# Performance work log

Hardware: AMD Instinct MI355X
Metric: run time of the kernel (lower is better)

The kernel has to match this reference:

```python
import jax, jax.numpy as jnp
import numpy as np

N_NODES = 50000
N_EDGES = 800000
NFEAT = 128
NHID = 128


def gcn_conv(x, edge_index, W, b):
    """PyG GCNConv: add self-loops, symmetric deg^-1/2 normalization, scatter-add."""
    n = x.shape[0]
    loop = jnp.arange(n, dtype=edge_index.dtype)
    row = jnp.concatenate([edge_index[0], loop])  # source nodes
    col = jnp.concatenate([edge_index[1], loop])  # target nodes
    ones = jnp.ones(row.shape[0], dtype=x.dtype)
    deg = jax.ops.segment_sum(ones, col, num_segments=n)
    dinv = jnp.where(deg > 0, jax.lax.rsqrt(deg), 0.0).astype(x.dtype)
    norm = dinv[row] * dinv[col]  # [E+N]
    h = x @ W  # [n, out]
    msg = h[row] * norm[:, None]  # gather + scale, [E+N, out]
    out = jax.ops.segment_sum(msg, col, num_segments=n)  # scatter-add
    return out + b


def setup_inputs() -> dict:
    key = jax.random.key(0)
    kx, ke, k1, k2 = jax.random.split(key, 4)
    x = jax.random.normal(kx, (N_NODES, NFEAT), dtype=jnp.float32)
    edge_index = jax.random.randint(ke, (2, N_EDGES), 0, N_NODES, dtype=jnp.int32)
    s1 = 1.0 / np.sqrt(NFEAT)
    s2 = 1.0 / np.sqrt(NHID)
    W1 = jax.random.uniform(k1, (NFEAT, NHID), jnp.float32, -s1, s1)
    b1 = jnp.zeros((NHID,), jnp.float32)
    W2 = jax.random.uniform(k2, (NHID, NHID), jnp.float32, -s2, s2)
    b2 = jnp.zeros((NHID,), jnp.float32)
    return {"x": x, "edge_index": edge_index, "W1": W1, "b1": b1, "W2": W2, "b2": b2}


def reference(x, edge_index, W1, b1, W2, b2):
    # DGI.forward -> encoder z: relu(GCNConv) x2, dropout=0, no layernorm
    h = jax.nn.relu(gcn_conv(x, edge_index, W1, b1))
    z = jax.nn.relu(gcn_conv(h, edge_index, W2, b2))
    return z
```

## Files before the change

kernel.cpp:

```cpp
#include <hip/hip_runtime.h>
#include <hip/hip_fp16.h>


#define NBK 98
#define BSH 9
#define BCAP 10240
#define NBB 391

typedef _Float16 f16x8 __attribute__((ext_vector_type(8)));
typedef float f32x4 __attribute__((ext_vector_type(4)));

__global__ __launch_bounds__(256) void k_prep_bucket(
    const int* __restrict__ row, const int* __restrict__ col,
    int* __restrict__ bcur, unsigned int* __restrict__ arena, int E,
    const float* __restrict__ W1, const float* __restrict__ W2,
    __half* __restrict__ Wt1, __half* __restrict__ Wt2) {
  int tid = threadIdx.x;
  if (blockIdx.x >= NBB) {
    int i = (blockIdx.x - NBB) * 256 + tid;
    int n = i >> 7, k = i & 127;
    Wt1[i] = (__half)W1[k * 128 + n];
    Wt2[i] = (__half)W2[k * 128 + n];
    return;
  }
  __shared__ int hist[NBK];
  __shared__ int basec[NBK];
  if (tid < NBK) hist[tid] = 0;
  __syncthreads();
  int base = blockIdx.x * 2048;
  int cc[8], rr[8], bb[8];
#pragma unroll
  for (int j = 0; j < 8; ++j) {
    int e = base + j * 256 + tid;
    bb[j] = -1;
    if (e < E) {
      cc[j] = col[e];
      rr[j] = row[e];
      bb[j] = cc[j] >> BSH;
      atomicAdd(&hist[bb[j]], 1);
    }
  }
  __syncthreads();
  if (tid < NBK && hist[tid] > 0)
    basec[tid] = atomicAdd(&bcur[tid], hist[tid]);
  __syncthreads();
#pragma unroll
  for (int j = 0; j < 8; ++j) {
    if (bb[j] >= 0) {
      int pos = atomicAdd(&basec[bb[j]], 1);
      if (pos < BCAP)
        arena[(size_t)bb[j] * BCAP + pos] =
            ((unsigned int)rr[j] << BSH) | (unsigned int)(cc[j] & 511);
    }
  }
}

__global__ __launch_bounds__(256) void k_csr(const int* __restrict__ bcur,
                                             const unsigned int* __restrict__ arena,
                                             int* __restrict__ offs,
                                             float* __restrict__ dinv,
                                             int* __restrict__ esrc, int n) {
  __shared__ int hist[512];
  __shared__ int psum[256];
  int b = blockIdx.x, tid = threadIdx.x;
  hist[tid] = 0;
  hist[tid + 256] = 0;
  __syncthreads();
  int m = min(bcur[b], BCAP);
  const unsigned int* a = arena + (size_t)b * BCAP;
  for (int i = tid; i < m; i += 256) atomicAdd(&hist[a[i] & 511], 1);
  __syncthreads();

  psum[tid] = (tid < b && tid < NBK) ? min(bcur[tid], BCAP) : 0;
  __syncthreads();
#pragma unroll
  for (int d = 128; d > 0; d >>= 1) {
    if (tid < d) psum[tid] += psum[tid + d];
    __syncthreads();
  }
  int base = psum[0];
  __syncthreads();

  int a0 = hist[2 * tid], a1 = hist[2 * tid + 1];
  int pair = a0 + a1;
  psum[tid] = pair;
  __syncthreads();
#pragma unroll
  for (int d = 1; d < 256; d <<= 1) {
    int add = (tid >= d) ? psum[tid - d] : 0;
    __syncthreads();
    psum[tid] += add;
    __syncthreads();
  }
  int excl = psum[tid] - pair;
  int o0 = base + excl, o1 = o0 + a0;

  int nb0 = b << BSH;
  int node0 = nb0 + 2 * tid, node1 = node0 + 1;
  if (node0 < n) {
    offs[node0] = o0;
    dinv[node0] = rsqrtf((float)(a0 + 1));
  }
  if (node1 < n) {
    offs[node1] = o1;
    dinv[node1] = rsqrtf((float)(a1 + 1));
  }
  if (b == NBK - 1 && tid == 255) offs[n] = base + psum[255];
  __syncthreads();

  hist[2 * tid] = o0;
  hist[2 * tid + 1] = o1;
  __syncthreads();
  for (int i = tid; i < m; i += 256) {
    unsigned int p = a[i];
    int pos = atomicAdd(&hist[p & 511], 1);
    esrc[pos] = (int)(p >> BSH);
  }
}

__device__ inline uint4 loadA16(const float* A, int grow, int k16, int M) {
  if (grow >= M) return make_uint4(0, 0, 0, 0);
  const float4* p = (const float4*)(A + (size_t)grow * 128 + k16 * 8);
  float4 f0 = p[0], f1 = p[1];
  __half2 h0 = __floats2half2_rn(f0.x, f0.y);
  __half2 h1 = __floats2half2_rn(f0.z, f0.w);
  __half2 h2 = __floats2half2_rn(f1.x, f1.y);
  __half2 h3 = __floats2half2_rn(f1.z, f1.w);
  uint4 u;
  u.x = *(unsigned int*)&h0;
  u.y = *(unsigned int*)&h1;
  u.z = *(unsigned int*)&h2;
  u.w = *(unsigned int*)&h3;
  return u;
}
__device__ inline uint4 loadA16(const __half* A, int grow, int k16, int M) {
  if (grow >= M) return make_uint4(0, 0, 0, 0);
  return *(const uint4*)(A + (size_t)grow * 128 + k16 * 8);
}

template <typename AT>
__global__ __launch_bounds__(256) void k_gemm(const AT* __restrict__ A,
                                              const __half* __restrict__ Wt,
                                              const float* __restrict__ dinv,
                                              __half* __restrict__ C, int M) {
  __shared__ char smem[16384 + 32768];
  char* Al = smem;
  char* Bl = smem + 16384;
  int tid = threadIdx.x;
  int row0 = blockIdx.x * 64;

  const uint4* Wt4 = (const uint4*)Wt;
#pragma unroll
  for (int i = 0; i < 8; ++i) {
    int c = tid + 256 * i;
    int n = c >> 4, k16 = c & 15;
    *(uint4*)(Bl + n * 256 + ((k16 * 16) ^ ((n & 7) << 4))) = Wt4[c];
  }
#pragma unroll
  for (int i = 0; i < 4; ++i) {
    int c = tid + 256 * i;
    int r = c >> 4, k16 = c & 15;
    uint4 v = loadA16(A, row0 + r, k16, M);
    *(uint4*)(Al + r * 256 + ((k16 * 16) ^ ((r & 7) << 4))) = v;
  }
  __syncthreads();

  int w = tid >> 6, l = tid & 63;
  int lr = l & 15, lq = l >> 4;
  f32x4 acc[8] = {};
#pragma unroll
  for (int kc = 0; kc < 4; ++kc) {
    int c16 = kc * 4 + lq;
    int ar = w * 16 + lr;
    f16x8 av = *(const f16x8*)(Al + ar * 256 + ((c16 * 16) ^ ((lr & 7) << 4)));
#pragma unroll
    for (int nt = 0; nt < 8; ++nt) {
      int n = nt * 16 + lr;
      f16x8 bv = *(const f16x8*)(Bl + n * 256 + ((c16 * 16) ^ ((n & 7) << 4)));
      acc[nt] = __builtin_amdgcn_mfma_f32_16x16x32_f16(av, bv, acc[nt], 0, 0, 0);
    }
  }

  int orow = row0 + w * 16 + lq * 4;
#pragma unroll
  for (int r = 0; r < 4; ++r) {
    int grow = orow + r;
    if (grow < M) {
      float dv = dinv[grow];
#pragma unroll
      for (int nt = 0; nt < 8; ++nt)
        C[(size_t)grow * 128 + nt * 16 + lr] = (__half)(acc[nt][r] * dv);
    }
  }
}

template <bool FP16OUT>
__global__ __launch_bounds__(256) void k_agg(const __half* __restrict__ hs,
                                             const int* __restrict__ offs,
                                             const int* __restrict__ esrc,
                                             const float* __restrict__ dinv,
                                             const float* __restrict__ bias,
                                             void* __restrict__ outp, int n) {
  int gw = (blockIdx.x * 256 + threadIdx.x) >> 6;
  int lane = threadIdx.x & 63;
  if (gw >= n) return;
  float di = dinv[gw];
  const unsigned int* base = (const unsigned int*)hs;
  unsigned int su = base[(size_t)gw * 64 + lane];
  float2 v = __half22float2(*(__half2*)&su);
  float ax = v.x, ay = v.y;
  int e0 = offs[gw], e1 = offs[gw + 1];
  int e = e0;
  for (; e + 16 <= e1; e += 16) {
    int s[16];
#pragma unroll
    for (int j = 0; j < 16; ++j) s[j] = esrc[e + j];
    unsigned int u[16];
#pragma unroll
    for (int j = 0; j < 16; ++j) u[j] = base[(size_t)s[j] * 64 + lane];
#pragma unroll
    for (int j = 0; j < 16; ++j) {
      float2 hv = __half22float2(*(__half2*)&u[j]);
      ax += hv.x;
      ay += hv.y;
    }
  }
  int cnt = e1 - e;
  if (cnt > 0) {
    int s[16];
#pragma unroll
    for (int j = 0; j < 16; ++j)
      if (j < cnt) s[j] = esrc[e + j];
    unsigned int u[16];
#pragma unroll
    for (int j = 0; j < 16; ++j)
      if (j < cnt) u[j] = base[(size_t)s[j] * 64 + lane];
#pragma unroll
    for (int j = 0; j < 16; ++j)
      if (j < cnt) {
        float2 hv = __half22float2(*(__half2*)&u[j]);
        ax += hv.x;
        ay += hv.y;
      }
  }
  float2 bv = ((const float2*)bias)[lane];
  float ox = fmaxf(fmaf(ax, di, bv.x), 0.f);
  float oy = fmaxf(fmaf(ay, di, bv.y), 0.f);
  if (FP16OUT) {
    __half2 p = __floats2half2_rn(ox, oy);
    ((unsigned int*)outp)[(size_t)gw * 64 + lane] = *(unsigned int*)&p;
  } else {
    ((float2*)outp)[(size_t)gw * 64 + lane] = make_float2(ox, oy);
  }
}

extern "C" void kernel_launch(void* const* d_in, const int* in_sizes, int n_in,
                              void* d_out, int out_size, void* d_ws, size_t ws_size,
                              hipStream_t stream) {
  const float* x  = (const float*)d_in[0];
  const int*   ei = (const int*)d_in[1];
  const float* W1 = (const float*)d_in[2];
  const float* b1 = (const float*)d_in[3];
  const float* W2 = (const float*)d_in[4];
  const float* b2 = (const float*)d_in[5];
  const int n = in_sizes[0] / 128;
  const int E = in_sizes[1] / 2;
  const int* row = ei;
  const int* col = ei + E;

  char* ws = (char*)d_ws;
  size_t off = 0;
  auto alloc = [&](size_t bytes) -> void* {
    void* p = ws + off;
    off = (off + bytes + 255) & ~(size_t)255;
    return p;
  };
  int*          offs  = (int*)alloc((size_t)(n + 1) * 4);
  float*        dinv  = (float*)alloc((size_t)n * 4);
  int*          bcur  = (int*)alloc(NBK * 4);
  int*          esrc  = (int*)alloc((size_t)E * 4);
  unsigned int* arena = (unsigned int*)alloc((size_t)NBK * BCAP * 4);
  __half*       Wt1   = (__half*)alloc(128 * 128 * 2);
  __half*       Wt2   = (__half*)alloc(128 * 128 * 2);
  __half*       hs1   = (__half*)alloc((size_t)n * 128 * 2);
  __half*       h16   = (__half*)alloc((size_t)n * 128 * 2);
  __half*       hs2   = (__half*)alloc((size_t)n * 128 * 2);
  (void)ws_size; (void)n_in; (void)out_size;

  hipMemsetAsync(bcur, 0, NBK * 4, stream);
  k_prep_bucket<<<NBB + 64, 256, 0, stream>>>(row, col, bcur, arena, E,
                                              W1, W2, Wt1, Wt2);
  k_csr<<<NBK, 256, 0, stream>>>(bcur, arena, offs, dinv, esrc, n);

  const int gb = (n + 63) / 64;
  const int ab = (n * 64 + 255) / 256;
  k_gemm<float><<<gb, 256, 0, stream>>>(x, Wt1, dinv, hs1, n);
  k_agg<true><<<ab, 256, 0, stream>>>(hs1, offs, esrc, dinv, b1, h16, n);
  k_gemm<__half><<<gb, 256, 0, stream>>>(h16, Wt2, dinv, hs2, n);
  k_agg<false><<<ab, 256, 0, stream>>>(hs2, offs, esrc, dinv, b2, d_out, n);
}
```

Measured before the change: 129.6 us.

## Fuse all GCN stages into one persistent cooperative kernel with grid syncs

```diff
diff --git a/kernel.cpp b/kernel.cpp
--- a/kernel.cpp
+++ b/kernel.cpp
@@ -1,122 +1,16 @@
 #include <hip/hip_runtime.h>
 #include <hip/hip_fp16.h>
+#include <hip/hip_cooperative_groups.h>
+
+namespace cg = cooperative_groups;
 
 
 #define NBK 98
 #define BSH 9
 #define BCAP 10240
-#define NBB 391
 
 typedef _Float16 f16x8 __attribute__((ext_vector_type(8)));
 typedef float f32x4 __attribute__((ext_vector_type(4)));
-
-__global__ __launch_bounds__(256) void k_prep_bucket(
-    const int* __restrict__ row, const int* __restrict__ col,
-    int* __restrict__ bcur, unsigned int* __restrict__ arena, int E,
-    const float* __restrict__ W1, const float* __restrict__ W2,
-    __half* __restrict__ Wt1, __half* __restrict__ Wt2) {
-  int tid = threadIdx.x;
-  if (blockIdx.x >= NBB) {
-    int i = (blockIdx.x - NBB) * 256 + tid;
-    int n = i >> 7, k = i & 127;
-    Wt1[i] = (__half)W1[k * 128 + n];
-    Wt2[i] = (__half)W2[k * 128 + n];
-    return;
-  }
-  __shared__ int hist[NBK];
-  __shared__ int basec[NBK];
-  if (tid < NBK) hist[tid] = 0;
-  __syncthreads();
-  int base = blockIdx.x * 2048;
-  int cc[8], rr[8], bb[8];
-#pragma unroll
-  for (int j = 0; j < 8; ++j) {
-    int e = base + j * 256 + tid;
-    bb[j] = -1;
-    if (e < E) {
-      cc[j] = col[e];
-      rr[j] = row[e];
-      bb[j] = cc[j] >> BSH;
-      atomicAdd(&hist[bb[j]], 1);
-    }
-  }
-  __syncthreads();
-  if (tid < NBK && hist[tid] > 0)
-    basec[tid] = atomicAdd(&bcur[tid], hist[tid]);
-  __syncthreads();
-#pragma unroll
-  for (int j = 0; j < 8; ++j) {
-    if (bb[j] >= 0) {
-      int pos = atomicAdd(&basec[bb[j]], 1);
-      if (pos < BCAP)
-        arena[(size_t)bb[j] * BCAP + pos] =
-            ((unsigned int)rr[j] << BSH) | (unsigned int)(cc[j] & 511);
-    }
-  }
-}
-
-__global__ __launch_bounds__(256) void k_csr(const int* __restrict__ bcur,
-                                             const unsigned int* __restrict__ arena,
-                                             int* __restrict__ offs,
-                                             float* __restrict__ dinv,
-                                             int* __restrict__ esrc, int n) {
-  __shared__ int hist[512];
-  __shared__ int psum[256];
-  int b = blockIdx.x, tid = threadIdx.x;
-  hist[tid] = 0;
-  hist[tid + 256] = 0;
-  __syncthreads();
-  int m = min(bcur[b], BCAP);
-  const unsigned int* a = arena + (size_t)b * BCAP;
-  for (int i = tid; i < m; i += 256) atomicAdd(&hist[a[i] & 511], 1);
-  __syncthreads();
-
-  psum[tid] = (tid < b && tid < NBK) ? min(bcur[tid], BCAP) : 0;
-  __syncthreads();
-#pragma unroll
-  for (int d = 128; d > 0; d >>= 1) {
-    if (tid < d) psum[tid] += psum[tid + d];
-    __syncthreads();
-  }
-  int base = psum[0];
-  __syncthreads();
-
-  int a0 = hist[2 * tid], a1 = hist[2 * tid + 1];
-  int pair = a0 + a1;
-  psum[tid] = pair;
-  __syncthreads();
-#pragma unroll
-  for (int d = 1; d < 256; d <<= 1) {
-    int add = (tid >= d) ? psum[tid - d] : 0;
-    __syncthreads();
-    psum[tid] += add;
-    __syncthreads();
-  }
-  int excl = psum[tid] - pair;
-  int o0 = base + excl, o1 = o0 + a0;
-
-  int nb0 = b << BSH;
-  int node0 = nb0 + 2 * tid, node1 = node0 + 1;
-  if (node0 < n) {
-    offs[node0] = o0;
-    dinv[node0] = rsqrtf((float)(a0 + 1));
-  }
-  if (node1 < n) {
-    offs[node1] = o1;
-    dinv[node1] = rsqrtf((float)(a1 + 1));
-  }
-  if (b == NBK - 1 && tid == 255) offs[n] = base + psum[255];
-  __syncthreads();
-
-  hist[2 * tid] = o0;
-  hist[2 * tid + 1] = o1;
-  __syncthreads();
-  for (int i = tid; i < m; i += 256) {
-    unsigned int p = a[i];
-    int pos = atomicAdd(&hist[p & 511], 1);
-    esrc[pos] = (int)(p >> BSH);
-  }
-}
 
 __device__ inline uint4 loadA16(const float* A, int grow, int k16, int M) {
   if (grow >= M) return make_uint4(0, 0, 0, 0);
@@ -139,119 +33,237 @@
 }
 
 template <typename AT>
-__global__ __launch_bounds__(256) void k_gemm(const AT* __restrict__ A,
-                                              const __half* __restrict__ Wt,
-                                              const float* __restrict__ dinv,
-                                              __half* __restrict__ C, int M) {
-  __shared__ char smem[16384 + 32768];
+__device__ void gemm_phase(const AT* __restrict__ A, const __half* __restrict__ Wt,
+                           const float* __restrict__ dinv, __half* __restrict__ C,
+                           int M, char* smem) {
   char* Al = smem;
   char* Bl = smem + 16384;
   int tid = threadIdx.x;
-  int row0 = blockIdx.x * 64;
-
   const uint4* Wt4 = (const uint4*)Wt;
-#pragma unroll
-  for (int i = 0; i < 8; ++i) {
-    int c = tid + 256 * i;
-    int n = c >> 4, k16 = c & 15;
-    *(uint4*)(Bl + n * 256 + ((k16 * 16) ^ ((n & 7) << 4))) = Wt4[c];
-  }
-#pragma unroll
-  for (int i = 0; i < 4; ++i) {
-    int c = tid + 256 * i;
-    int r = c >> 4, k16 = c & 15;
-    uint4 v = loadA16(A, row0 + r, k16, M);
-    *(uint4*)(Al + r * 256 + ((k16 * 16) ^ ((r & 7) << 4))) = v;
-  }
-  __syncthreads();
-
-  int w = tid >> 6, l = tid & 63;
-  int lr = l & 15, lq = l >> 4;
-  f32x4 acc[8] = {};
-#pragma unroll
-  for (int kc = 0; kc < 4; ++kc) {
-    int c16 = kc * 4 + lq;
-    int ar = w * 16 + lr;
-    f16x8 av = *(const f16x8*)(Al + ar * 256 + ((c16 * 16) ^ ((lr & 7) << 4)));
-#pragma unroll
-    for (int nt = 0; nt < 8; ++nt) {
-      int n = nt * 16 + lr;
-      f16x8 bv = *(const f16x8*)(Bl + n * 256 + ((c16 * 16) ^ ((n & 7) << 4)));
-      acc[nt] = __builtin_amdgcn_mfma_f32_16x16x32_f16(av, bv, acc[nt], 0, 0, 0);
-    }
-  }
-
-  int orow = row0 + w * 16 + lq * 4;
-#pragma unroll
-  for (int r = 0; r < 4; ++r) {
-    int grow = orow + r;
-    if (grow < M) {
-      float dv = dinv[grow];
-#pragma unroll
-      for (int nt = 0; nt < 8; ++nt)
-        C[(size_t)grow * 128 + nt * 16 + lr] = (__half)(acc[nt][r] * dv);
+  int ntile = (M + 63) / 64;
+  for (int t = blockIdx.x; t < ntile; t += gridDim.x) {
+    __syncthreads();
+#pragma unroll
+    for (int i = 0; i < 4; ++i) {
+      int c = tid + 512 * i;
+      int nn = c >> 4, k16 = c & 15;
+      *(uint4*)(Bl + nn * 256 + ((k16 * 16) ^ ((nn & 7) << 4))) = Wt4[c];
+    }
+    int row0 = t * 64;
+#pragma unroll
+    for (int i = 0; i < 2; ++i) {
+      int c = tid + 512 * i;
+      int r = c >> 4, k16 = c & 15;
+      uint4 v = loadA16(A, row0 + r, k16, M);
+      *(uint4*)(Al + r * 256 + ((k16 * 16) ^ ((r & 7) << 4))) = v;
+    }
+    __syncthreads();
+    int w = tid >> 6, l = tid & 63;
+    int wr = w & 3, wn = w >> 2;
+    int lr = l & 15, lq = l >> 4;
+    f32x4 acc[4] = {};
+#pragma unroll
+    for (int kc = 0; kc < 4; ++kc) {
+      int c16 = kc * 4 + lq;
+      int ar = wr * 16 + lr;
+      f16x8 av = *(const f16x8*)(Al + ar * 256 + ((c16 * 16) ^ ((lr & 7) << 4)));
+#pragma unroll
+      for (int ntl = 0; ntl < 4; ++ntl) {
+        int nn = (wn * 4 + ntl) * 16 + lr;
+        f16x8 bv = *(const f16x8*)(Bl + nn * 256 + ((c16 * 16) ^ ((nn & 7) << 4)));
+        acc[ntl] = __builtin_amdgcn_mfma_f32_16x16x32_f16(av, bv, acc[ntl], 0, 0, 0);
+      }
+    }
+    int orow = row0 + wr * 16 + lq * 4;
+#pragma unroll
+    for (int r = 0; r < 4; ++r) {
+      int grow = orow + r;
+      if (grow < M) {
+        float dv = dinv[grow];
+#pragma unroll
+        for (int ntl = 0; ntl < 4; ++ntl)
+          C[(size_t)grow * 128 + (wn * 4 + ntl) * 16 + lr] =
+              (__half)(acc[ntl][r] * dv);
+      }
     }
   }
 }
 
 template <bool FP16OUT>
-__global__ __launch_bounds__(256) void k_agg(const __half* __restrict__ hs,
-                                             const int* __restrict__ offs,
-                                             const int* __restrict__ esrc,
-                                             const float* __restrict__ dinv,
-                                             const float* __restrict__ bias,
-                                             void* __restrict__ outp, int n) {
-  int gw = (blockIdx.x * 256 + threadIdx.x) >> 6;
+__device__ void agg_phase(const __half* __restrict__ hs, const int* __restrict__ offs,
+                          const int* __restrict__ esrc, const float* __restrict__ dinv,
+                          const float* __restrict__ bias, void* __restrict__ outp,
+                          int n) {
   int lane = threadIdx.x & 63;
-  if (gw >= n) return;
-  float di = dinv[gw];
+  int gw0 = blockIdx.x * 8 + (threadIdx.x >> 6);
+  int gstride = gridDim.x * 8;
   const unsigned int* base = (const unsigned int*)hs;
-  unsigned int su = base[(size_t)gw * 64 + lane];
-  float2 v = __half22float2(*(__half2*)&su);
-  float ax = v.x, ay = v.y;
-  int e0 = offs[gw], e1 = offs[gw + 1];
-  int e = e0;
-  for (; e + 16 <= e1; e += 16) {
-    int s[16];
-#pragma unroll
-    for (int j = 0; j < 16; ++j) s[j] = esrc[e + j];
-    unsigned int u[16];
-#pragma unroll
-    for (int j = 0; j < 16; ++j) u[j] = base[(size_t)s[j] * 64 + lane];
-#pragma unroll
-    for (int j = 0; j < 16; ++j) {
-      float2 hv = __half22float2(*(__half2*)&u[j]);
-      ax += hv.x;
-      ay += hv.y;
-    }
-  }
-  int cnt = e1 - e;
-  if (cnt > 0) {
-    int s[16];
-#pragma unroll
-    for (int j = 0; j < 16; ++j)
-      if (j < cnt) s[j] = esrc[e + j];
-    unsigned int u[16];
-#pragma unroll
-    for (int j = 0; j < 16; ++j)
-      if (j < cnt) u[j] = base[(size_t)s[j] * 64 + lane];
-#pragma unroll
-    for (int j = 0; j < 16; ++j)
-      if (j < cnt) {
+  float2 bv = ((const float2*)bias)[lane];
+  for (int gw = gw0; gw < n; gw += gstride) {
+    float di = dinv[gw];
+    unsigned int su = base[(size_t)gw * 64 + lane];
+    float2 v = __half22float2(*(__half2*)&su);
+    float ax = v.x, ay = v.y;
+    int e0 = offs[gw], e1 = offs[gw + 1];
+    int e = e0;
+    for (; e + 16 <= e1; e += 16) {
+      int s[16];
+#pragma unroll
+      for (int j = 0; j < 16; ++j) s[j] = esrc[e + j];
+      unsigned int u[16];
+#pragma unroll
+      for (int j = 0; j < 16; ++j) u[j] = base[(size_t)s[j] * 64 + lane];
+#pragma unroll
+      for (int j = 0; j < 16; ++j) {
         float2 hv = __half22float2(*(__half2*)&u[j]);
         ax += hv.x;
         ay += hv.y;
       }
-  }
-  float2 bv = ((const float2*)bias)[lane];
-  float ox = fmaxf(fmaf(ax, di, bv.x), 0.f);
-  float oy = fmaxf(fmaf(ay, di, bv.y), 0.f);
-  if (FP16OUT) {
-    __half2 p = __floats2half2_rn(ox, oy);
-    ((unsigned int*)outp)[(size_t)gw * 64 + lane] = *(unsigned int*)&p;
-  } else {
-    ((float2*)outp)[(size_t)gw * 64 + lane] = make_float2(ox, oy);
-  }
+    }
+    int cnt = e1 - e;
+    if (cnt > 0) {
+      int s[16];
+#pragma unroll
+      for (int j = 0; j < 16; ++j)
+        if (j < cnt) s[j] = esrc[e + j];
+      unsigned int u[16];
+#pragma unroll
+      for (int j = 0; j < 16; ++j)
+        if (j < cnt) u[j] = base[(size_t)s[j] * 64 + lane];
+#pragma unroll
+      for (int j = 0; j < 16; ++j)
+        if (j < cnt) {
+          float2 hv = __half22float2(*(__half2*)&u[j]);
+          ax += hv.x;
+          ay += hv.y;
+        }
+    }
+    float ox = fmaxf(fmaf(ax, di, bv.x), 0.f);
+    float oy = fmaxf(fmaf(ay, di, bv.y), 0.f);
+    if (FP16OUT) {
+      __half2 p = __floats2half2_rn(ox, oy);
+      ((unsigned int*)outp)[(size_t)gw * 64 + lane] = *(unsigned int*)&p;
+    } else {
+      ((float2*)outp)[(size_t)gw * 64 + lane] = make_float2(ox, oy);
+    }
+  }
+}
+
+__global__ __launch_bounds__(512, 4) void k_mega(
+    const int* __restrict__ row, const int* __restrict__ col, int E,
+    const float* __restrict__ x, const float* __restrict__ W1,
+    const float* __restrict__ b1, const float* __restrict__ W2,
+    const float* __restrict__ b2, int* __restrict__ bcur,
+    unsigned int* __restrict__ arena, int* __restrict__ offs,
+    float* __restrict__ dinv, int* __restrict__ esrc,
+    __half* __restrict__ Wt1, __half* __restrict__ Wt2,
+    __half* __restrict__ hs1, __half* __restrict__ h16,
+    __half* __restrict__ hs2, float* __restrict__ out, int n) {
+  cg::grid_group grid = cg::this_grid();
+  __shared__ alignas(16) char smem[49152];
+  int tid = threadIdx.x;
+  int bid = blockIdx.x;
+  int nblk = gridDim.x;
+
+  for (int i = bid * 512 + tid; i < 16384; i += nblk * 512) {
+    int nn = i >> 7, k = i & 127;
+    Wt1[i] = (__half)W1[k * 128 + nn];
+    Wt2[i] = (__half)W2[k * 128 + nn];
+  }
+  for (int i = bid * 512 + tid; i < NBK; i += nblk * 512) bcur[i] = 0;
+  grid.sync();
+
+  {
+    int* hist = (int*)smem;
+    int* basec = hist + 128;
+    int nchunk = (E + 2047) / 2048;
+    for (int c = bid; c < nchunk; c += nblk) {
+      __syncthreads();
+      if (tid < NBK) hist[tid] = 0;
+      __syncthreads();
+      int base = c * 2048;
+      int cc[4], rr[4], bb[4];
+#pragma unroll
+      for (int j = 0; j < 4; ++j) {
+        int e = base + j * 512 + tid;
+        bb[j] = -1;
+        if (e < E) {
+          cc[j] = col[e];
+          rr[j] = row[e];
+          bb[j] = cc[j] >> BSH;
+          atomicAdd(&hist[bb[j]], 1);
+        }
+      }
+      __syncthreads();
+      if (tid < NBK && hist[tid] > 0)
+        basec[tid] = atomicAdd(&bcur[tid], hist[tid]);
+      __syncthreads();
+#pragma unroll
+      for (int j = 0; j < 4; ++j) {
+        if (bb[j] >= 0) {
+          int pos = atomicAdd(&basec[bb[j]], 1);
+          if (pos < BCAP)
+            arena[(size_t)bb[j] * BCAP + pos] =
+                ((unsigned int)rr[j] << BSH) | (unsigned int)(cc[j] & 511);
+        }
+      }
+    }
+  }
+  grid.sync();
+
+  {
+    int* hist = (int*)smem;
+    int* scan = hist + 512;
+    int* bsh = scan + 512;
+    for (int b = bid; b < NBK; b += nblk) {
+      __syncthreads();
+      hist[tid] = 0;
+      if (tid < 128) bsh[tid] = (tid < NBK) ? min(bcur[tid], BCAP) : 0;
+      __syncthreads();
+      int m = bsh[b];
+      const unsigned int* a = arena + (size_t)b * BCAP;
+      for (int i = tid; i < m; i += 512) atomicAdd(&hist[a[i] & 511], 1);
+      __syncthreads();
+      int base = 0;
+      for (int t = 0; t < b; ++t) base += bsh[t];
+      int v = hist[tid];
+      scan[tid] = v;
+      __syncthreads();
+      for (int d = 1; d < 512; d <<= 1) {
+        int add = (tid >= d) ? scan[tid - d] : 0;
+        __syncthreads();
+        scan[tid] += add;
+        __syncthreads();
+      }
+      int o = base + scan[tid] - v;
+      int node = (b << BSH) + tid;
+      if (node < n) {
+        offs[node] = o;
+        dinv[node] = rsqrtf((float)(v + 1));
+      }
+      if (b == NBK - 1 && tid == 511) offs[n] = base + scan[511];
+      __syncthreads();
+      hist[tid] = o;
+      __syncthreads();
+      for (int i = tid; i < m; i += 512) {
+        unsigned int p = a[i];
+        int pos = atomicAdd(&hist[p & 511], 1);
+        esrc[pos] = (int)(p >> BSH);
+      }
+    }
+  }
+  grid.sync();
+
+  gemm_phase<float>(x, Wt1, dinv, hs1, n, smem);
+  grid.sync();
+
+  agg_phase<true>(hs1, offs, esrc, dinv, b1, h16, n);
+  grid.sync();
+
+  gemm_phase<__half>(h16, Wt2, dinv, hs2, n, smem);
+  grid.sync();
+
+  agg_phase<false>(hs2, offs, esrc, dinv, b2, out, n);
 }
 
 extern "C" void kernel_launch(void* const* d_in, const int* in_sizes, int n_in,
@@ -263,8 +275,8 @@
   const float* b1 = (const float*)d_in[3];
   const float* W2 = (const float*)d_in[4];
   const float* b2 = (const float*)d_in[5];
-  const int n = in_sizes[0] / 128;
-  const int E = in_sizes[1] / 2;
+  int n = in_sizes[0] / 128;
+  int E = in_sizes[1] / 2;
   const int* row = ei;
   const int* col = ei + E;
 
@@ -285,17 +297,19 @@
   __half*       hs1   = (__half*)alloc((size_t)n * 128 * 2);
   __half*       h16   = (__half*)alloc((size_t)n * 128 * 2);
   __half*       hs2   = (__half*)alloc((size_t)n * 128 * 2);
+  float*        outp  = (float*)d_out;
   (void)ws_size; (void)n_in; (void)out_size;
 
-  hipMemsetAsync(bcur, 0, NBK * 4, stream);
-  k_prep_bucket<<<NBB + 64, 256, 0, stream>>>(row, col, bcur, arena, E,
-                                              W1, W2, Wt1, Wt2);
-  k_csr<<<NBK, 256, 0, stream>>>(bcur, arena, offs, dinv, esrc, n);
-
-  const int gb = (n + 63) / 64;
-  const int ab = (n * 64 + 255) / 256;
-  k_gemm<float><<<gb, 256, 0, stream>>>(x, Wt1, dinv, hs1, n);
-  k_agg<true><<<ab, 256, 0, stream>>>(hs1, offs, esrc, dinv, b1, h16, n);
-  k_gemm<__half><<<gb, 256, 0, stream>>>(h16, Wt2, dinv, hs2, n);
-  k_agg<false><<<ab, 256, 0, stream>>>(hs2, offs, esrc, dinv, b2, d_out, n);
-}
+  int occ = 0;
+  hipOccupancyMaxActiveBlocksPerMultiprocessor(&occ, k_mega, 512, 0);
+  if (occ < 1) occ = 1;
+  if (occ > 3) occ = 3;
+  dim3 grid(occ * 256), block(512);
+
+  void* args[] = {(void*)&row, (void*)&col, (void*)&E,    (void*)&x,
+                  (void*)&W1,  (void*)&b1,  (void*)&W2,   (void*)&b2,
+                  (void*)&bcur,(void*)&arena,(void*)&offs,(void*)&dinv,
+                  (void*)&esrc,(void*)&Wt1, (void*)&Wt2,  (void*)&hs1,
+                  (void*)&h16, (void*)&hs2, (void*)&outp, (void*)&n};
+  hipLaunchCooperativeKernel(k_mega, grid, block, args, 0, stream);
+}
```

After: 340.3 us. 2.63x slower.

## Fuse bucket, CSR build and memset into one cooperative kernel with grid syncs

Applied to the files above, without the earlier changes.

```diff
diff --git a/kernel.cpp b/kernel.cpp
--- a/kernel.cpp
+++ b/kernel.cpp
@@ -1,5 +1,8 @@
 #include <hip/hip_runtime.h>
 #include <hip/hip_fp16.h>
+#include <hip/hip_cooperative_groups.h>
+
+namespace cg = cooperative_groups;
 
 
 #define NBK 98
@@ -10,111 +13,121 @@
 typedef _Float16 f16x8 __attribute__((ext_vector_type(8)));
 typedef float f32x4 __attribute__((ext_vector_type(4)));
 
-__global__ __launch_bounds__(256) void k_prep_bucket(
-    const int* __restrict__ row, const int* __restrict__ col,
-    int* __restrict__ bcur, unsigned int* __restrict__ arena, int E,
+__global__ __launch_bounds__(256) void k_build(
+    const int* __restrict__ row, const int* __restrict__ col, int E,
     const float* __restrict__ W1, const float* __restrict__ W2,
-    __half* __restrict__ Wt1, __half* __restrict__ Wt2) {
-  int tid = threadIdx.x;
-  if (blockIdx.x >= NBB) {
-    int i = (blockIdx.x - NBB) * 256 + tid;
-    int n = i >> 7, k = i & 127;
-    Wt1[i] = (__half)W1[k * 128 + n];
-    Wt2[i] = (__half)W2[k * 128 + n];
-    return;
-  }
-  __shared__ int hist[NBK];
-  __shared__ int basec[NBK];
-  if (tid < NBK) hist[tid] = 0;
-  __syncthreads();
-  int base = blockIdx.x * 2048;
-  int cc[8], rr[8], bb[8];
-#pragma unroll
-  for (int j = 0; j < 8; ++j) {
-    int e = base + j * 256 + tid;
-    bb[j] = -1;
-    if (e < E) {
-      cc[j] = col[e];
-      rr[j] = row[e];
-      bb[j] = cc[j] >> BSH;
-      atomicAdd(&hist[bb[j]], 1);
-    }
-  }
-  __syncthreads();
-  if (tid < NBK && hist[tid] > 0)
-    basec[tid] = atomicAdd(&bcur[tid], hist[tid]);
-  __syncthreads();
-#pragma unroll
-  for (int j = 0; j < 8; ++j) {
-    if (bb[j] >= 0) {
-      int pos = atomicAdd(&basec[bb[j]], 1);
-      if (pos < BCAP)
-        arena[(size_t)bb[j] * BCAP + pos] =
-            ((unsigned int)rr[j] << BSH) | (unsigned int)(cc[j] & 511);
-    }
-  }
-}
-
-__global__ __launch_bounds__(256) void k_csr(const int* __restrict__ bcur,
-                                             const unsigned int* __restrict__ arena,
-                                             int* __restrict__ offs,
-                                             float* __restrict__ dinv,
-                                             int* __restrict__ esrc, int n) {
+    __half* __restrict__ Wt1, __half* __restrict__ Wt2,
+    int* __restrict__ bcur, unsigned int* __restrict__ arena,
+    int* __restrict__ offs, float* __restrict__ dinv,
+    int* __restrict__ esrc, int n) {
+  cg::grid_group grid = cg::this_grid();
   __shared__ int hist[512];
   __shared__ int psum[256];
-  int b = blockIdx.x, tid = threadIdx.x;
-  hist[tid] = 0;
-  hist[tid + 256] = 0;
-  __syncthreads();
-  int m = min(bcur[b], BCAP);
-  const unsigned int* a = arena + (size_t)b * BCAP;
-  for (int i = tid; i < m; i += 256) atomicAdd(&hist[a[i] & 511], 1);
-  __syncthreads();
-
-  psum[tid] = (tid < b && tid < NBK) ? min(bcur[tid], BCAP) : 0;
-  __syncthreads();
-#pragma unroll
-  for (int d = 128; d > 0; d >>= 1) {
-    if (tid < d) psum[tid] += psum[tid + d];
-    __syncthreads();
-  }
-  int base = psum[0];
-  __syncthreads();
-
-  int a0 = hist[2 * tid], a1 = hist[2 * tid + 1];
-  int pair = a0 + a1;
-  psum[tid] = pair;
-  __syncthreads();
-#pragma unroll
-  for (int d = 1; d < 256; d <<= 1) {
-    int add = (tid >= d) ? psum[tid - d] : 0;
-    __syncthreads();
-    psum[tid] += add;
-    __syncthreads();
-  }
-  int excl = psum[tid] - pair;
-  int o0 = base + excl, o1 = o0 + a0;
-
-  int nb0 = b << BSH;
-  int node0 = nb0 + 2 * tid, node1 = node0 + 1;
-  if (node0 < n) {
-    offs[node0] = o0;
-    dinv[node0] = rsqrtf((float)(a0 + 1));
-  }
-  if (node1 < n) {
-    offs[node1] = o1;
-    dinv[node1] = rsqrtf((float)(a1 + 1));
-  }
-  if (b == NBK - 1 && tid == 255) offs[n] = base + psum[255];
-  __syncthreads();
-
-  hist[2 * tid] = o0;
-  hist[2 * tid + 1] = o1;
-  __syncthreads();
-  for (int i = tid; i < m; i += 256) {
-    unsigned int p = a[i];
-    int pos = atomicAdd(&hist[p & 511], 1);
-    esrc[pos] = (int)(p >> BSH);
+  int tid = threadIdx.x;
+  int bid = blockIdx.x;
+  int nblk = gridDim.x;
+
+  for (int i = bid * 256 + tid; i < 16384; i += nblk * 256) {
+    int nn = i >> 7, k = i & 127;
+    Wt1[i] = (__half)W1[k * 128 + nn];
+    Wt2[i] = (__half)W2[k * 128 + nn];
+  }
+  if (bid == 0 && tid < NBK) bcur[tid] = 0;
+  grid.sync();
+
+  {
+    int* bhist = hist;
+    int* basec = hist + 128;
+    int nchunk = (E + 2047) / 2048;
+    for (int c = bid; c < nchunk; c += nblk) {
+      __syncthreads();
+      if (tid < NBK) bhist[tid] = 0;
+      __syncthreads();
+      int base = c * 2048;
+      int cc[8], rr[8], bb[8];
+#pragma unroll
+      for (int j = 0; j < 8; ++j) {
+        int e = base + j * 256 + tid;
+        bb[j] = -1;
+        if (e < E) {
+          cc[j] = col[e];
+          rr[j] = row[e];
+          bb[j] = cc[j] >> BSH;
+          atomicAdd(&bhist[bb[j]], 1);
+        }
+      }
+      __syncthreads();
+      if (tid < NBK && bhist[tid] > 0)
+        basec[tid] = atomicAdd(&bcur[tid], bhist[tid]);
+      __syncthreads();
+#pragma unroll
+      for (int j = 0; j < 8; ++j) {
+        if (bb[j] >= 0) {
+          int pos = atomicAdd(&basec[bb[j]], 1);
+          if (pos < BCAP)
+            arena[(size_t)bb[j] * BCAP + pos] =
+                ((unsigned int)rr[j] << BSH) | (unsigned int)(cc[j] & 511);
+        }
+      }
+    }
+  }
+  grid.sync();
+
+  for (int b = bid; b < NBK; b += nblk) {
+    __syncthreads();
+    hist[tid] = 0;
+    hist[tid + 256] = 0;
+    __syncthreads();
+    int m = min(bcur[b], BCAP);
+    const unsigned int* a = arena + (size_t)b * BCAP;
+    for (int i = tid; i < m; i += 256) atomicAdd(&hist[a[i] & 511], 1);
+    __syncthreads();
+
+    psum[tid] = (tid < b && tid < NBK) ? min(bcur[tid], BCAP) : 0;
+    __syncthreads();
+#pragma unroll
+    for (int d = 128; d > 0; d >>= 1) {
+      if (tid < d) psum[tid] += psum[tid + d];
+      __syncthreads();
+    }
+    int base = psum[0];
+    __syncthreads();
+
+    int a0 = hist[2 * tid], a1 = hist[2 * tid + 1];
+    int pair = a0 + a1;
+    psum[tid] = pair;
+    __syncthreads();
+#pragma unroll
+    for (int d = 1; d < 256; d <<= 1) {
+      int add = (tid >= d) ? psum[tid - d] : 0;
+      __syncthreads();
+      psum[tid] += add;
+      __syncthreads();
+    }
+    int excl = psum[tid] - pair;
+    int o0 = base + excl, o1 = o0 + a0;
+
+    int nb0 = b << BSH;
+    int node0 = nb0 + 2 * tid, node1 = node0 + 1;
+    if (node0 < n) {
+      offs[node0] = o0;
+      dinv[node0] = rsqrtf((float)(a0 + 1));
+    }
+    if (node1 < n) {
+      offs[node1] = o1;
+      dinv[node1] = rsqrtf((float)(a1 + 1));
+    }
+    if (b == NBK - 1 && tid == 255) offs[n] = base + psum[255];
+    __syncthreads();
+
+    hist[2 * tid] = o0;
+    hist[2 * tid + 1] = o1;
+    __syncthreads();
+    for (int i = tid; i < m; i += 256) {
+      unsigned int p = a[i];
+      int pos = atomicAdd(&hist[p & 511], 1);
+      esrc[pos] = (int)(p >> BSH);
+    }
   }
 }
 
@@ -263,8 +276,8 @@
   const float* b1 = (const float*)d_in[3];
   const float* W2 = (const float*)d_in[4];
   const float* b2 = (const float*)d_in[5];
-  const int n = in_sizes[0] / 128;
-  const int E = in_sizes[1] / 2;
+  int n = in_sizes[0] / 128;
+  int E = in_sizes[1] / 2;
   const int* row = ei;
   const int* col = ei + E;
 
@@ -287,10 +300,11 @@
   __half*       hs2   = (__half*)alloc((size_t)n * 128 * 2);
   (void)ws_size; (void)n_in; (void)out_size;
 
-  hipMemsetAsync(bcur, 0, NBK * 4, stream);
-  k_prep_bucket<<<NBB + 64, 256, 0, stream>>>(row, col, bcur, arena, E,
-                                              W1, W2, Wt1, Wt2);
-  k_csr<<<NBK, 256, 0, stream>>>(bcur, arena, offs, dinv, esrc, n);
+  void* bargs[] = {(void*)&row, (void*)&col, (void*)&E,    (void*)&W1,
+                   (void*)&W2,  (void*)&Wt1, (void*)&Wt2,  (void*)&bcur,
+                   (void*)&arena,(void*)&offs,(void*)&dinv,(void*)&esrc,
+                   (void*)&n};
+  hipLaunchCooperativeKernel(k_build, dim3(NBB), dim3(256), bargs, 0, stream);
 
   const int gb = (n + 63) / 64;
   const int ab = (n * 64 + 255) / 256;
```

New measurement: 220.0 us. 69.7% more time.
